# Performance work log

Measured on AMD Instinct MI355X. Metric: run time of the kernel, lower is better.

The kernel has to match this reference:

```python
import jax, jax.numpy as jnp
import numpy as np

T, D, I, E, G, LG, K = 2048, 1024, 512, 32, 8, 4, 6
SI = 2 * I  # shared expert inter dim = n_shared_experts * inter_dim
ROUTE_SCALE = 1.0


def setup_inputs() -> dict:
    key = jax.random.key(0)
    ks = jax.random.split(key, 16)
    s = 0.02
    f = jnp.float32
    return {
        "x": jax.random.normal(ks[0], (T, D), f),
        "router_w": jax.random.normal(ks[1], (E, D), f) * s,
        "router_b": jax.random.normal(ks[2], (E,), f) * s,
        "W1": jax.random.normal(ks[3], (E, D, I), f) * s,
        "b1": jax.random.normal(ks[4], (E, I), f) * s,
        "W2": jax.random.normal(ks[5], (E, D, I), f) * s,
        "b2": jax.random.normal(ks[6], (E, I), f) * s,
        "W3": jax.random.normal(ks[7], (E, I, D), f) * s,
        "b3": jax.random.normal(ks[8], (E, D), f) * s,
        "sw1": jax.random.normal(ks[9], (D, SI), f) * s,
        "sb1": jax.random.normal(ks[10], (SI,), f) * s,
        "sw2": jax.random.normal(ks[11], (D, SI), f) * s,
        "sb2": jax.random.normal(ks[12], (SI,), f) * s,
        "sw3": jax.random.normal(ks[13], (SI, D), f) * s,
        "sb3": jax.random.normal(ks[14], (D,), f) * s,
    }


def _route(x, router_w, router_b):
    # Router: softmax scores (fp32), group-limited top-k.
    logits = x @ router_w.T + router_b                      # [T, E]
    scores = jax.nn.softmax(logits.astype(jnp.float32), axis=-1)
    original = scores
    sg = scores.reshape(x.shape[0], G, E // G)              # [T, G, E/G]
    # no router bias -> group score = sum of top-2 expert scores per group
    group_scores = jnp.sum(jax.lax.top_k(sg, 2)[0], axis=-1)  # [T, G]
    _, gidx = jax.lax.top_k(group_scores, LG)               # [T, LG]
    keep = jnp.zeros((x.shape[0], G), bool).at[jnp.arange(x.shape[0])[:, None], gidx].set(True)
    masked = jnp.where(keep[:, :, None], sg, -jnp.inf).reshape(x.shape[0], E)
    _, idx = jax.lax.top_k(masked, K)                       # [T, K]
    vals = jnp.take_along_axis(original, idx, axis=1) * ROUTE_SCALE
    return vals.astype(x.dtype), idx


def reference(x, router_w, router_b, W1, b1, W2, b2, W3, b3, sw1, sb1, sw2, sb2, sw3, sb3):
    vals, idx = _route(x, router_w, router_b)
    # dense gate matrix [T, E]; top-k indices per row are distinct
    gates = jnp.zeros((x.shape[0], E), x.dtype).at[jnp.arange(x.shape[0])[:, None], idx].set(vals)
    # routed experts: Expert(x) = W3 @ silu(w1(x) * w2(x))
    h1 = jnp.einsum('td,edi->tei', x, W1) + b1              # [T, E, I]
    h2 = jnp.einsum('td,edi->tei', x, W2) + b2
    h = jax.nn.silu(h1 * h2)
    y = jnp.einsum('tei,eid->td', h * gates[:, :, None], W3) + gates @ b3
    # shared expert
    z = jax.nn.silu((x @ sw1 + sb1) * (x @ sw2 + sb2)) @ sw3 + sb3
    return y + z
```

## Files before the change

### kernel.cpp

```cpp
#include <hip/hip_runtime.h>
#include <hip/hip_bf16.h>
#include <math.h>

#define T_CONST 2048
#define D_CONST 1024
#define I_CONST 512
#define SI_CONST 1024
#define E_CONST 32
#define G_CONST 8
#define LG_CONST 4
#define KSEL 6
#define BK 32

typedef __attribute__((ext_vector_type(8))) short short8;
typedef __attribute__((ext_vector_type(4))) float floatx4;

__device__ inline unsigned pack_bf16(float a, float b) {
  __hip_bfloat162 h = __float22bfloat162_rn(float2{a, b});
  return *reinterpret_cast<unsigned*>(&h);
}

__device__ inline void gload16(const void* g, void* l) {
  __builtin_amdgcn_global_load_lds(
      (const __attribute__((address_space(1))) unsigned int*)g,
      (__attribute__((address_space(3))) unsigned int*)l, 16, 0, 0);
}

__global__ __launch_bounds__(256) void prep_all(
    const float* __restrict__ x, const float* __restrict__ rw,
    const float* __restrict__ W1, const float* __restrict__ W2,
    const float* __restrict__ W3, const float* __restrict__ sw1,
    const float* __restrict__ sw2, const float* __restrict__ sw3,
    __hip_bfloat16* __restrict__ x_bf, float* __restrict__ rwt,
    __hip_bfloat16* __restrict__ W1t, __hip_bfloat16* __restrict__ W2t,
    __hip_bfloat16* __restrict__ W3t, __hip_bfloat16* __restrict__ sw1t,
    __hip_bfloat16* __restrict__ sw2t, __hip_bfloat16* __restrict__ sw3t) {
  const int b = blockIdx.x;
  const int tid = threadIdx.x;
  if (b >= 3264) {
    int lb = b - 3264;
    if (lb < 512) {
      size_t base = (size_t)lb * 4096 + tid * 4;
#pragma unroll
      for (int it = 0; it < 4; ++it) {
        float4 v = *(const float4*)&x[base + it * 1024];
        uint2 u{pack_bf16(v.x, v.y), pack_bf16(v.z, v.w)};
        *(uint2*)&x_bf[base + it * 1024] = u;
      }
    } else {
      int lb2 = lb - 512;
#pragma unroll
      for (int it = 0; it < 4; ++it) {
        int i = lb2 * 1024 + it * 256 + tid;
        int d = i >> 5, e = i & 31;
        rwt[d * 32 + e] = rw[e * D_CONST + d];
      }
    }
    return;
  }
  const float* in;
  __hip_bfloat16* out;
  int K, N, k0, n0;
  if (b < 2048) {
    int mat = b >> 5, rem = b & 31;
    K = 1024; N = 512;
    int e = mat & 31;
    in = ((mat < 32) ? W1 : W2) + (size_t)e * (1024 * 512);
    out = ((mat < 32) ? W1t : W2t) + (size_t)e * (1024 * 512);
    k0 = (rem >> 3) * 256; n0 = (rem & 7) * 64;
  } else if (b < 3072) {
    int local = b - 2048;
    int e = local >> 5, rem = local & 31;
    K = 512; N = 1024;
    in = W3 + (size_t)e * (512 * 1024);
    out = W3t + (size_t)e * (512 * 1024);
    k0 = (rem >> 4) * 256; n0 = (rem & 15) * 64;
  } else {
    int local = b - 3072;
    int which = local >> 6, rem = local & 63;
    K = 1024; N = 1024;
    in = which == 0 ? sw1 : which == 1 ? sw2 : sw3;
    out = which == 0 ? sw1t : which == 1 ? sw2t : sw3t;
    k0 = (rem >> 4) * 256; n0 = (rem & 15) * 64;
  }
  __shared__ short tile[64 * 256];
  const int u = tid & 15, tr = tid >> 4;
#pragma unroll
  for (int sub = 0; sub < 4; ++sub) {
    float4 v[4];
#pragma unroll
    for (int r = 0; r < 4; ++r)
      v[r] = *(const float4*)&in[(size_t)(k0 + sub * 64 + 4 * tr + r) * N + n0 + 4 * u];
    int kb = sub * 64 + 4 * tr;
    int chunk = kb >> 3, half = (kb >> 2) & 1;
#pragma unroll
    for (int j = 0; j < 4; ++j) {
      int n = 4 * u + j;
      unsigned lo = pack_bf16(((const float*)&v[0])[j], ((const float*)&v[1])[j]);
      unsigned hi = pack_bf16(((const float*)&v[2])[j], ((const float*)&v[3])[j]);
      int cx = chunk ^ ((n >> 2) & 7) ^ ((n & 3) << 3);
      *(uint2*)&tile[n * 256 + cx * 8 + half * 4] = uint2{lo, hi};
    }
  }
  __syncthreads();
  const int n_ = tid >> 5, c_ = tid & 31;
#pragma unroll
  for (int p = 0; p < 8; ++p) {
    int n = p * 8 + n_;
    int cx = c_ ^ ((n >> 2) & 7) ^ ((n & 3) << 3);
    uint4 o = *(const uint4*)&tile[n * 256 + cx * 8];
    *(uint4*)&out[(size_t)(n0 + n) * K + k0 + c_ * 8] = o;
  }
}

__global__ __launch_bounds__(256) void router2(
    const float* __restrict__ x, const float* __restrict__ rwt,
    const float* __restrict__ rb, int* __restrict__ counts,
    int* __restrict__ stok, float* __restrict__ gatel) {
  const int lane = threadIdx.x & 63;
  const int wv = threadIdx.x >> 6;
  const int t = blockIdx.x * 4 + wv;
  const int e = lane & 31, h = lane >> 5;
  const float* xp = x + (size_t)t * D_CONST;
  float s = 0.f;
#pragma unroll 8
  for (int d = h; d < D_CONST; d += 2) s = fmaf(xp[d], rwt[d * 32 + e], s);
  s += __shfl_xor(s, 32);
  s += rb[e];
  float mx = s;
#pragma unroll
  for (int m = 16; m >= 1; m >>= 1) mx = fmaxf(mx, __shfl_xor(mx, m));
  float p = expf(s - mx);
  float sum = p;
#pragma unroll
  for (int m = 16; m >= 1; m >>= 1) sum += __shfl_xor(sum, m);
  float sc = p / sum;
  float a = sc, bb = __shfl_xor(a, 1);
  float hi = fmaxf(a, bb), lo = fminf(a, bb);
  float oh = __shfl_xor(hi, 2), ol = __shfl_xor(lo, 2);
  float gs = fmaxf(fmaxf(hi + oh, hi + lo), oh + ol);
  const int g = e >> 2;
  unsigned keep = 0;
  float gv = gs;
#pragma unroll
  for (int r = 0; r < LG_CONST; ++r) {
    float v = gv;
    int gi = g;
#pragma unroll
    for (int m = 16; m >= 1; m >>= 1) {
      float ov = __shfl_xor(v, m);
      int og = __shfl_xor(gi, m);
      if (ov > v || (ov == v && og < gi)) { v = ov; gi = og; }
    }
    keep |= 1u << gi;
    if (g == gi) gv = -1e30f;
  }
  float cand = ((keep >> g) & 1u) ? sc : -1e30f;
  int sel_e = -1;
  float sel_v = 0.f;
#pragma unroll
  for (int r = 0; r < KSEL; ++r) {
    float v = cand;
    int ei = e;
#pragma unroll
    for (int m = 16; m >= 1; m >>= 1) {
      float ov = __shfl_xor(v, m);
      int oe = __shfl_xor(ei, m);
      if (ov > v || (ov == v && oe < ei)) { v = ov; ei = oe; }
    }
    if (lane == r) { sel_e = ei; sel_v = v; }
    if (e == ei) cand = -1e30f;
  }
  if (lane < KSEL) {
    int pos = atomicAdd(&counts[sel_e], 1);
    stok[sel_e * T_CONST + pos] = t;
    gatel[sel_e * T_CONST + pos] = sel_v;
  }
}

__global__ __launch_bounds__(64) void plan_build(
    const int* __restrict__ counts, int* __restrict__ offsets,
    int* __restrict__ plan_up, int* __restrict__ plan_dn, int* __restrict__ meta) {
  const int lane = threadIdx.x;
  for (int i = lane; i < 128; i += 64) {
    int ent = (E_CONST << 8) | i;
    plan_up[i] = ent;
    plan_dn[i] = ent;
  }
  int cnt = (lane < E_CONST) ? counts[lane] : 0;
  int incl = cnt;
#pragma unroll
  for (int d = 1; d < 64; d <<= 1) {
    int v = __shfl_up(incl, d);
    if (lane >= d) incl += v;
  }
  if (lane < E_CONST) offsets[lane] = incl - cnt;
  if (lane == E_CONST - 1) offsets[E_CONST] = incl;
  int mbs = (cnt + 127) >> 7;
  int pm = mbs;
#pragma unroll
  for (int d = 1; d < 64; d <<= 1) {
    int v = __shfl_up(pm, d);
    if (lane >= d) pm += v;
  }
  int pmex = pm - mbs;
  if (lane < E_CONST) {
    int ub = 128 + pmex * 4, db = 128 + pmex * 8;
    for (int mb = 0; mb < mbs; ++mb) {
#pragma unroll
      for (int nb = 0; nb < 4; ++nb)
        plan_up[ub + mb * 4 + nb] = (lane << 8) | (mb << 3) | nb;
#pragma unroll
      for (int nb = 0; nb < 8; ++nb)
        plan_dn[db + mb * 8 + nb] = (lane << 8) | (mb << 3) | nb;
    }
  }
  if (lane == E_CONST - 1) {
    meta[0] = 128 + pm * 4;
    meta[1] = 128 + pm * 8;
  }
}

__global__ __launch_bounds__(256) void gather_x(
    const __hip_bfloat16* __restrict__ xbf, const int* __restrict__ counts,
    const int* __restrict__ offsets, const int* __restrict__ stok,
    const float* __restrict__ gatel, __hip_bfloat16* __restrict__ Xg,
    float* __restrict__ cgate, int* __restrict__ tcnt, int* __restrict__ tslot) {
  int e = blockIdx.x;
  int cnt = counts[e];
  int row = blockIdx.y * 16 + (threadIdx.x >> 4);
  if (row >= cnt) return;
  int seg = threadIdx.x & 15;
  int tok = stok[e * T_CONST + row];
  int dst = offsets[e] + row;
  const uint4* src = (const uint4*)(xbf + (size_t)tok * D_CONST);
  uint4* d = (uint4*)(Xg + (size_t)dst * D_CONST);
#pragma unroll
  for (int i = 0; i < 8; ++i) d[i * 16 + seg] = src[i * 16 + seg];
  if (seg == 0) {
    cgate[dst] = gatel[e * T_CONST + row];
    int sl = atomicAdd(&tcnt[tok], 1);
    tslot[tok * 8 + sl] = dst;
  }
}

__global__ __launch_bounds__(256, 2) void up_fused(
    const __hip_bfloat16* __restrict__ Xg, const __hip_bfloat16* __restrict__ xbf,
    const __hip_bfloat16* __restrict__ W1t, const __hip_bfloat16* __restrict__ W2t,
    const __hip_bfloat16* __restrict__ sw1t, const __hip_bfloat16* __restrict__ sw2t,
    const float* __restrict__ b1, const float* __restrict__ b2,
    const float* __restrict__ sb1, const float* __restrict__ sb2,
    const int* __restrict__ counts, const int* __restrict__ offsets,
    const int* __restrict__ plan, const int* __restrict__ meta,
    __hip_bfloat16* __restrict__ He, __hip_bfloat16* __restrict__ Hs) {
  const int nw = meta[0];
  const int bx = blockIdx.x;
  if (bx >= nw) return;
  const int q = nw >> 3, r = nw & 7, c = bx & 7, sl = bx >> 3;
  const int j = (c < r ? c * (q + 1) : r * (q + 1) + (c - r) * q) + sl;
  const int ent = plan[j];
  const int z = ent >> 8;
  const int m0 = ((ent >> 3) & 31) * 128;
  const int n0 = (ent & 7) * 128;
  const bool SH = (z == E_CONST);
  const int cnt = SH ? T_CONST : counts[z];
  const int base = SH ? 0 : offsets[z];

  const __hip_bfloat16* Ab = SH ? (xbf + (size_t)m0 * D_CONST)
                                : (Xg + (size_t)(base + m0) * D_CONST);
  const __hip_bfloat16* B1 = SH ? (sw1t + (size_t)n0 * D_CONST)
                                : (W1t + ((size_t)z * I_CONST + n0) * D_CONST);
  const __hip_bfloat16* B2 = SH ? (sw2t + (size_t)n0 * D_CONST)
                                : (W2t + ((size_t)z * I_CONST + n0) * D_CONST);

  __shared__ short As[3 * 4096], Bs1[3 * 4096], Bs2[3 * 4096];

  const int tid = threadIdx.x, lane = tid & 63, wv = tid >> 6;
  const int l15 = lane & 15, quad = lane >> 4;
  const int wm = wv & 1, wn = wv >> 1;
  const int lr = lane >> 2;
  const int lc = lane & 3;

  const __hip_bfloat16 *aG[2], *b1G[2], *b2G[2];
#pragma unroll
  for (int i = 0; i < 2; ++i) {
    int rr = wv * 32 + i * 16 + lr;
    int kap = lc ^ ((rr >> 1) & 3);
    aG[i]  = Ab + (size_t)rr * D_CONST + kap * 8;
    b1G[i] = B1 + (size_t)rr * D_CONST + kap * 8;
    b2G[i] = B2 + (size_t)rr * D_CONST + kap * 8;
  }
  const int ldsu = wv * 1024 + lane * 8;

  floatx4 acc1[4][4] = {};
  floatx4 acc2[4][4] = {};

  const int nIter = D_CONST / BK;

  auto stage = [&](int slot, int kk) {
    const int sb = slot * 4096;
#pragma unroll
    for (int i = 0; i < 2; ++i) {
      gload16(aG[i] + kk,  &As [sb + ldsu + i * 512]);
      gload16(b1G[i] + kk, &Bs1[sb + ldsu + i * 512]);
      gload16(b2G[i] + kk, &Bs2[sb + ldsu + i * 512]);
    }
  };

  stage(0, 0);
  stage(1, BK);
  int sl0 = 0, sl1 = 1, sl2 = 2;

  for (int s = 0; s < nIter; ++s) {
    int kn = (s + 2 < nIter) ? (s + 2) * BK : (nIter - 1) * BK;
    stage(sl2, kn);
    asm volatile("s_waitcnt vmcnt(12)" ::: "memory");
    __builtin_amdgcn_s_barrier();
    const int sb = sl0 * 4096;
    short8 a[4], x1[4], x2[4];
#pragma unroll
    for (int mi = 0; mi < 4; ++mi) {
      int m = wm * 64 + mi * 16 + l15;
      a[mi] = *(const short8*)&As[sb + m * 32 + (quad ^ ((m >> 1) & 3)) * 8];
    }
#pragma unroll
    for (int ni = 0; ni < 4; ++ni) {
      int n = wn * 64 + ni * 16 + l15;
      int uo = sb + n * 32 + (quad ^ ((n >> 1) & 3)) * 8;
      x1[ni] = *(const short8*)&Bs1[uo];
      x2[ni] = *(const short8*)&Bs2[uo];
    }
    __builtin_amdgcn_s_setprio(1);
#pragma unroll
    for (int mi = 0; mi < 4; ++mi)
#pragma unroll
      for (int ni = 0; ni < 4; ++ni) {
        acc1[mi][ni] = __builtin_amdgcn_mfma_f32_16x16x32_bf16(a[mi], x1[ni], acc1[mi][ni], 0, 0, 0);
        acc2[mi][ni] = __builtin_amdgcn_mfma_f32_16x16x32_bf16(a[mi], x2[ni], acc2[mi][ni], 0, 0, 0);
      }
    __builtin_amdgcn_s_setprio(0);
    __builtin_amdgcn_s_barrier();
    int t = sl0; sl0 = sl1; sl1 = sl2; sl2 = t;
  }
  asm volatile("s_waitcnt vmcnt(0)" ::: "memory");

  const float* pb1 = SH ? sb1 : (b1 + (size_t)z * I_CONST);
  const float* pb2 = SH ? sb2 : (b2 + (size_t)z * I_CONST);
  __hip_bfloat16* outp = SH ? (Hs + (size_t)m0 * SI_CONST + n0)
                            : (He + (size_t)(base + m0) * I_CONST + n0);
  const int ldo = SH ? SI_CONST : I_CONST;
  float c1[4], c2[4];
#pragma unroll
  for (int ni = 0; ni < 4; ++ni) {
    int n = wn * 64 + ni * 16 + l15;
    c1[ni] = pb1[n0 + n];
    c2[ni] = pb2[n0 + n];
  }
#pragma unroll
  for (int mi = 0; mi < 4; ++mi) {
#pragma unroll
    for (int reg = 0; reg < 4; ++reg) {
      int m = wm * 64 + mi * 16 + quad * 4 + reg;
      if (m0 + m >= cnt) continue;
#pragma unroll
      for (int ni = 0; ni < 4; ++ni) {
        int n = wn * 64 + ni * 16 + l15;
        float h1 = acc1[mi][ni][reg] + c1[ni];
        float h2 = acc2[mi][ni][reg] + c2[ni];
        float p = h1 * h2;
        float sg = p / (1.f + expf(-p));
        outp[(size_t)m * ldo + n] = __float2bfloat16(sg);
      }
    }
  }
}

__global__ __launch_bounds__(256, 3) void down_fused(
    const __hip_bfloat16* __restrict__ He, const __hip_bfloat16* __restrict__ Hs,
    const __hip_bfloat16* __restrict__ W3t, const __hip_bfloat16* __restrict__ sw3t,
    const float* __restrict__ b3, const float* __restrict__ sb3,
    const int* __restrict__ counts, const int* __restrict__ offsets,
    const float* __restrict__ cgate, const int* __restrict__ plan,
    const int* __restrict__ meta, float* __restrict__ Yp, float* __restrict__ out) {
  if ((int)blockIdx.x >= meta[1]) return;
  const int ent = plan[blockIdx.x];
  const int z = ent >> 8;
  const int m0 = ((ent >> 3) & 31) * 128;
  const int n0 = (ent & 7) * 128;
  const bool SH = (z == E_CONST);
  const int cnt = SH ? T_CONST : counts[z];
  const int base = SH ? 0 : offsets[z];
  const int Kd = SH ? SI_CONST : I_CONST;

  const __hip_bfloat16* Ab = SH ? (Hs + (size_t)m0 * SI_CONST)
                                : (He + (size_t)(base + m0) * I_CONST);
  const __hip_bfloat16* Bb = SH ? (sw3t + (size_t)n0 * SI_CONST)
                                : (W3t + ((size_t)z * D_CONST + n0) * I_CONST);

  __shared__ short As[2 * 4096], Bs[2 * 4096];

  const int tid = threadIdx.x, lane = tid & 63, wv = tid >> 6;
  const int l15 = lane & 15, quad = lane >> 4;
  const int wm = wv & 1, wn = wv >> 1;
  const int lr = lane >> 2, lc = lane & 3;

  const __hip_bfloat16 *aG[2], *bG[2];
#pragma unroll
  for (int i = 0; i < 2; ++i) {
    int rr = wv * 32 + i * 16 + lr;
    int kap = lc ^ ((rr >> 1) & 3);
    aG[i] = Ab + (size_t)rr * Kd + kap * 8;
    bG[i] = Bb + (size_t)rr * Kd + kap * 8;
  }
  const int ldsu = wv * 1024 + lane * 8;

  floatx4 acc[4][4] = {};
  const int nIter = Kd / BK;

  auto stage = [&](int slot, int kk) {
    const int sb = slot * 4096;
#pragma unroll
    for (int i = 0; i < 2; ++i) {
      gload16(aG[i] + kk, &As[sb + ldsu + i * 512]);
      gload16(bG[i] + kk, &Bs[sb + ldsu + i * 512]);
    }
  };

  stage(0, 0);
  int cur = 0;

  for (int s = 0; s < nIter; ++s) {
    int kn = (s + 1 < nIter) ? (s + 1) * BK : s * BK;
    stage(cur ^ 1, kn);
    asm volatile("s_waitcnt vmcnt(4)" ::: "memory");
    __builtin_amdgcn_s_barrier();
    const int sb = cur * 4096;
    short8 a[4], bbf[4];
#pragma unroll
    for (int mi = 0; mi < 4; ++mi) {
      int m = wm * 64 + mi * 16 + l15;
      a[mi] = *(const short8*)&As[sb + m * 32 + (quad ^ ((m >> 1) & 3)) * 8];
    }
#pragma unroll
    for (int ni = 0; ni < 4; ++ni) {
      int n = wn * 64 + ni * 16 + l15;
      bbf[ni] = *(const short8*)&Bs[sb + n * 32 + (quad ^ ((n >> 1) & 3)) * 8];
    }
    __builtin_amdgcn_s_setprio(1);
#pragma unroll
    for (int mi = 0; mi < 4; ++mi)
#pragma unroll
      for (int ni = 0; ni < 4; ++ni)
        acc[mi][ni] = __builtin_amdgcn_mfma_f32_16x16x32_bf16(a[mi], bbf[ni], acc[mi][ni], 0, 0, 0);
    __builtin_amdgcn_s_setprio(0);
    __builtin_amdgcn_s_barrier();
    cur ^= 1;
  }
  asm volatile("s_waitcnt vmcnt(0)" ::: "memory");

  float bias[4];
#pragma unroll
  for (int ni = 0; ni < 4; ++ni) {
    int n = n0 + wn * 64 + ni * 16 + l15;
    bias[ni] = SH ? sb3[n] : b3[(size_t)z * D_CONST + n];
  }
#pragma unroll
  for (int mi = 0; mi < 4; ++mi) {
#pragma unroll
    for (int reg = 0; reg < 4; ++reg) {
      int m = wm * 64 + mi * 16 + quad * 4 + reg;
      if (m0 + m >= cnt) continue;
#pragma unroll
      for (int ni = 0; ni < 4; ++ni) {
        int n = n0 + wn * 64 + ni * 16 + l15;
        float v = acc[mi][ni][reg] + bias[ni];
        if (SH) {
          out[(size_t)(m0 + m) * D_CONST + n] = v;
        } else {
          int grow = base + m0 + m;
          Yp[(size_t)grow * D_CONST + n] = cgate[grow] * v;
        }
      }
    }
  }
}

__global__ __launch_bounds__(256) void combine(
    const float* __restrict__ Yp, const int* __restrict__ tslot,
    float* __restrict__ out) {
  const int t = blockIdx.x;
  const int d = threadIdx.x * 4;
  const int* ts = &tslot[t * 8];
  float4 o = *(const float4*)&out[(size_t)t * D_CONST + d];
#pragma unroll
  for (int k = 0; k < KSEL; ++k) {
    float4 y = *(const float4*)&Yp[(size_t)ts[k] * D_CONST + d];
    o.x += y.x; o.y += y.y; o.z += y.z; o.w += y.w;
  }
  *(float4*)&out[(size_t)t * D_CONST + d] = o;
}

extern "C" void kernel_launch(void* const* d_in, const int* in_sizes, int n_in,
                              void* d_out, int out_size, void* d_ws, size_t ws_size,
                              hipStream_t stream) {
  const float* x   = (const float*)d_in[0];
  const float* rw  = (const float*)d_in[1];
  const float* rb  = (const float*)d_in[2];
  const float* W1  = (const float*)d_in[3];
  const float* b1  = (const float*)d_in[4];
  const float* W2  = (const float*)d_in[5];
  const float* b2  = (const float*)d_in[6];
  const float* W3  = (const float*)d_in[7];
  const float* b3  = (const float*)d_in[8];
  const float* sw1 = (const float*)d_in[9];
  const float* sb1 = (const float*)d_in[10];
  const float* sw2 = (const float*)d_in[11];
  const float* sb2 = (const float*)d_in[12];
  const float* sw3 = (const float*)d_in[13];
  const float* sb3 = (const float*)d_in[14];
  float* out = (float*)d_out;

  char* w = (char*)d_ws;
  size_t off = 0;
  auto alloc = [&](size_t bytes) {
    char* p = w + off;
    off += (bytes + 255) & ~(size_t)255;
    return p;
  };
  int* counts = (int*)alloc(E_CONST * 4);
  int* offsets = (int*)alloc((E_CONST + 1) * 4);
  int* meta = (int*)alloc(16);
  int* plan_up = (int*)alloc(768 * 4);
  int* plan_dn = (int*)alloc(1280 * 4);
  int* tcnt = (int*)alloc((size_t)T_CONST * 4);
  int* tslot = (int*)alloc((size_t)T_CONST * 8 * 4);
  int* stok = (int*)alloc((size_t)E_CONST * T_CONST * 4);
  float* gatel = (float*)alloc((size_t)E_CONST * T_CONST * 4);
  float* rwt = (float*)alloc((size_t)D_CONST * E_CONST * 4);
  float* cgate = (float*)alloc((size_t)T_CONST * KSEL * 4);
  __hip_bfloat16* x_bf = (__hip_bfloat16*)alloc((size_t)T_CONST * D_CONST * 2);
  __hip_bfloat16* Xg = (__hip_bfloat16*)alloc((size_t)(T_CONST * KSEL + 128) * D_CONST * 2);
  __hip_bfloat16* W1t = (__hip_bfloat16*)alloc((size_t)E_CONST * D_CONST * I_CONST * 2);
  __hip_bfloat16* W2t = (__hip_bfloat16*)alloc((size_t)E_CONST * D_CONST * I_CONST * 2);
  __hip_bfloat16* W3t = (__hip_bfloat16*)alloc((size_t)E_CONST * I_CONST * D_CONST * 2);
  __hip_bfloat16* sw1t = (__hip_bfloat16*)alloc((size_t)D_CONST * SI_CONST * 2);
  __hip_bfloat16* sw2t = (__hip_bfloat16*)alloc((size_t)D_CONST * SI_CONST * 2);
  __hip_bfloat16* sw3t = (__hip_bfloat16*)alloc((size_t)SI_CONST * D_CONST * 2);
  __hip_bfloat16* He = (__hip_bfloat16*)alloc((size_t)(T_CONST * KSEL + 128) * I_CONST * 2);
  __hip_bfloat16* Hs = (__hip_bfloat16*)alloc((size_t)T_CONST * SI_CONST * 2);
  float* Yp = (float*)W1t;

  hipMemsetAsync(counts, 0, E_CONST * sizeof(int), stream);
  hipMemsetAsync(tcnt, 0, (size_t)T_CONST * sizeof(int), stream);
  prep_all<<<3808, 256, 0, stream>>>(x, rw, W1, W2, W3, sw1, sw2, sw3,
                                     x_bf, rwt, W1t, W2t, W3t, sw1t, sw2t, sw3t);
  router2<<<T_CONST / 4, 256, 0, stream>>>(x, rwt, rb, counts, stok, gatel);
  plan_build<<<1, 64, 0, stream>>>(counts, offsets, plan_up, plan_dn, meta);
  gather_x<<<dim3(E_CONST, T_CONST / 16), 256, 0, stream>>>(
      x_bf, counts, offsets, stok, gatel, Xg, cgate, tcnt, tslot);
  up_fused<<<768, 256, 0, stream>>>(
      Xg, x_bf, W1t, W2t, sw1t, sw2t, b1, b2, sb1, sb2, counts, offsets,
      plan_up, meta, He, Hs);
  down_fused<<<1280, 256, 0, stream>>>(
      He, Hs, W3t, sw3t, b3, sb3, counts, offsets, cgate, plan_dn, meta, Yp, out);
  combine<<<T_CONST, 256, 0, stream>>>(Yp, tslot, out);
}
```

Before: 459.4 us.

## Use 8-wave 512-thread blocks for up and down GEMM kernels

Doubles the block size of the up and down expert GEMM kernels from 4 to 8 waves while keeping the 128x128 output tile. Each wave now computes 64x32 instead of 64x64, which halves the accumulator registers. Each thread issues a single global-to-LDS load per operand per stage, and the vmcnt waits are adjusted to match. The intent is more resident waves per CU to hide memory latency. The trade-off is less register-level reuse of A fragments, since each A fragment now feeds only two MFMAs per operand, and more barrier participants per block.

```diff
diff --git a/kernel.cpp b/kernel.cpp
--- a/kernel.cpp
+++ b/kernel.cpp
@@ -244,7 +244,7 @@
   }
 }
 
-__global__ __launch_bounds__(256, 2) void up_fused(
+__global__ __launch_bounds__(512, 4) void up_fused(
     const __hip_bfloat16* __restrict__ Xg, const __hip_bfloat16* __restrict__ xbf,
     const __hip_bfloat16* __restrict__ W1t, const __hip_bfloat16* __restrict__ W2t,
     const __hip_bfloat16* __restrict__ sw1t, const __hip_bfloat16* __restrict__ sw2t,
@@ -278,33 +278,25 @@
   const int tid = threadIdx.x, lane = tid & 63, wv = tid >> 6;
   const int l15 = lane & 15, quad = lane >> 4;
   const int wm = wv & 1, wn = wv >> 1;
-  const int lr = lane >> 2;
-  const int lc = lane & 3;
-
-  const __hip_bfloat16 *aG[2], *b1G[2], *b2G[2];
-#pragma unroll
-  for (int i = 0; i < 2; ++i) {
-    int rr = wv * 32 + i * 16 + lr;
-    int kap = lc ^ ((rr >> 1) & 3);
-    aG[i]  = Ab + (size_t)rr * D_CONST + kap * 8;
-    b1G[i] = B1 + (size_t)rr * D_CONST + kap * 8;
-    b2G[i] = B2 + (size_t)rr * D_CONST + kap * 8;
-  }
-  const int ldsu = wv * 1024 + lane * 8;
-
-  floatx4 acc1[4][4] = {};
-  floatx4 acc2[4][4] = {};
+  const int srow = tid >> 2;
+  const int slc = tid & 3;
+  const int kap = slc ^ ((srow >> 1) & 3);
+
+  const __hip_bfloat16* aG  = Ab + (size_t)srow * D_CONST + kap * 8;
+  const __hip_bfloat16* b1G = B1 + (size_t)srow * D_CONST + kap * 8;
+  const __hip_bfloat16* b2G = B2 + (size_t)srow * D_CONST + kap * 8;
+  const int ldsu = tid * 8;
+
+  floatx4 acc1[4][2] = {};
+  floatx4 acc2[4][2] = {};
 
   const int nIter = D_CONST / BK;
 
   auto stage = [&](int slot, int kk) {
     const int sb = slot * 4096;
-#pragma unroll
-    for (int i = 0; i < 2; ++i) {
-      gload16(aG[i] + kk,  &As [sb + ldsu + i * 512]);
-      gload16(b1G[i] + kk, &Bs1[sb + ldsu + i * 512]);
-      gload16(b2G[i] + kk, &Bs2[sb + ldsu + i * 512]);
-    }
+    gload16(aG + kk,  &As [sb + ldsu]);
+    gload16(b1G + kk, &Bs1[sb + ldsu]);
+    gload16(b2G + kk, &Bs2[sb + ldsu]);
   };
 
   stage(0, 0);
@@ -314,30 +306,28 @@
   for (int s = 0; s < nIter; ++s) {
     int kn = (s + 2 < nIter) ? (s + 2) * BK : (nIter - 1) * BK;
     stage(sl2, kn);
-    asm volatile("s_waitcnt vmcnt(12)" ::: "memory");
+    asm volatile("s_waitcnt vmcnt(6)" ::: "memory");
     __builtin_amdgcn_s_barrier();
     const int sb = sl0 * 4096;
-    short8 a[4], x1[4], x2[4];
-#pragma unroll
-    for (int mi = 0; mi < 4; ++mi) {
-      int m = wm * 64 + mi * 16 + l15;
-      a[mi] = *(const short8*)&As[sb + m * 32 + (quad ^ ((m >> 1) & 3)) * 8];
-    }
-#pragma unroll
-    for (int ni = 0; ni < 4; ++ni) {
-      int n = wn * 64 + ni * 16 + l15;
+    short8 x1[2], x2[2];
+#pragma unroll
+    for (int ni = 0; ni < 2; ++ni) {
+      int n = wn * 32 + ni * 16 + l15;
       int uo = sb + n * 32 + (quad ^ ((n >> 1) & 3)) * 8;
       x1[ni] = *(const short8*)&Bs1[uo];
       x2[ni] = *(const short8*)&Bs2[uo];
     }
     __builtin_amdgcn_s_setprio(1);
 #pragma unroll
-    for (int mi = 0; mi < 4; ++mi)
-#pragma unroll
-      for (int ni = 0; ni < 4; ++ni) {
-        acc1[mi][ni] = __builtin_amdgcn_mfma_f32_16x16x32_bf16(a[mi], x1[ni], acc1[mi][ni], 0, 0, 0);
-        acc2[mi][ni] = __builtin_amdgcn_mfma_f32_16x16x32_bf16(a[mi], x2[ni], acc2[mi][ni], 0, 0, 0);
+    for (int mi = 0; mi < 4; ++mi) {
+      int m = wm * 64 + mi * 16 + l15;
+      short8 a = *(const short8*)&As[sb + m * 32 + (quad ^ ((m >> 1) & 3)) * 8];
+#pragma unroll
+      for (int ni = 0; ni < 2; ++ni) {
+        acc1[mi][ni] = __builtin_amdgcn_mfma_f32_16x16x32_bf16(a, x1[ni], acc1[mi][ni], 0, 0, 0);
+        acc2[mi][ni] = __builtin_amdgcn_mfma_f32_16x16x32_bf16(a, x2[ni], acc2[mi][ni], 0, 0, 0);
       }
+    }
     __builtin_amdgcn_s_setprio(0);
     __builtin_amdgcn_s_barrier();
     int t = sl0; sl0 = sl1; sl1 = sl2; sl2 = t;
@@ -349,10 +339,10 @@
   __hip_bfloat16* outp = SH ? (Hs + (size_t)m0 * SI_CONST + n0)
                             : (He + (size_t)(base + m0) * I_CONST + n0);
   const int ldo = SH ? SI_CONST : I_CONST;
-  float c1[4], c2[4];
-#pragma unroll
-  for (int ni = 0; ni < 4; ++ni) {
-    int n = wn * 64 + ni * 16 + l15;
+  float c1[2], c2[2];
+#pragma unroll
+  for (int ni = 0; ni < 2; ++ni) {
+    int n = wn * 32 + ni * 16 + l15;
     c1[ni] = pb1[n0 + n];
     c2[ni] = pb2[n0 + n];
   }
@@ -363,8 +353,8 @@
       int m = wm * 64 + mi * 16 + quad * 4 + reg;
       if (m0 + m >= cnt) continue;
 #pragma unroll
-      for (int ni = 0; ni < 4; ++ni) {
-        int n = wn * 64 + ni * 16 + l15;
+      for (int ni = 0; ni < 2; ++ni) {
+        int n = wn * 32 + ni * 16 + l15;
         float h1 = acc1[mi][ni][reg] + c1[ni];
         float h2 = acc2[mi][ni][reg] + c2[ni];
         float p = h1 * h2;
@@ -375,7 +365,7 @@
   }
 }
 
-__global__ __launch_bounds__(256, 3) void down_fused(
+__global__ __launch_bounds__(512, 4) void down_fused(
     const __hip_bfloat16* __restrict__ He, const __hip_bfloat16* __restrict__ Hs,
     const __hip_bfloat16* __restrict__ W3t, const __hip_bfloat16* __restrict__ sw3t,
     const float* __restrict__ b3, const float* __restrict__ sb3,
@@ -402,28 +392,20 @@
   const int tid = threadIdx.x, lane = tid & 63, wv = tid >> 6;
   const int l15 = lane & 15, quad = lane >> 4;
   const int wm = wv & 1, wn = wv >> 1;
-  const int lr = lane >> 2, lc = lane & 3;
-
-  const __hip_bfloat16 *aG[2], *bG[2];
-#pragma unroll
-  for (int i = 0; i < 2; ++i) {
-    int rr = wv * 32 + i * 16 + lr;
-    int kap = lc ^ ((rr >> 1) & 3);
-    aG[i] = Ab + (size_t)rr * Kd + kap * 8;
-    bG[i] = Bb + (size_t)rr * Kd + kap * 8;
-  }
-  const int ldsu = wv * 1024 + lane * 8;
-
-  floatx4 acc[4][4] = {};
+  const int srow = tid >> 2, slc = tid & 3;
+  const int kap = slc ^ ((srow >> 1) & 3);
+
+  const __hip_bfloat16* aG = Ab + (size_t)srow * Kd + kap * 8;
+  const __hip_bfloat16* bG = Bb + (size_t)srow * Kd + kap * 8;
+  const int ldsu = tid * 8;
+
+  floatx4 acc[4][2] = {};
   const int nIter = Kd / BK;
 
   auto stage = [&](int slot, int kk) {
     const int sb = slot * 4096;
-#pragma unroll
-    for (int i = 0; i < 2; ++i) {
-      gload16(aG[i] + kk, &As[sb + ldsu + i * 512]);
-      gload16(bG[i] + kk, &Bs[sb + ldsu + i * 512]);
-    }
+    gload16(aG + kk, &As[sb + ldsu]);
+    gload16(bG + kk, &Bs[sb + ldsu]);
   };
 
   stage(0, 0);
@@ -432,36 +414,34 @@
   for (int s = 0; s < nIter; ++s) {
     int kn = (s + 1 < nIter) ? (s + 1) * BK : s * BK;
     stage(cur ^ 1, kn);
-    asm volatile("s_waitcnt vmcnt(4)" ::: "memory");
+    asm volatile("s_waitcnt vmcnt(2)" ::: "memory");
     __builtin_amdgcn_s_barrier();
     const int sb = cur * 4096;
-    short8 a[4], bbf[4];
+    short8 bb[2];
+#pragma unroll
+    for (int ni = 0; ni < 2; ++ni) {
+      int n = wn * 32 + ni * 16 + l15;
+      bb[ni] = *(const short8*)&Bs[sb + n * 32 + (quad ^ ((n >> 1) & 3)) * 8];
+    }
+    __builtin_amdgcn_s_setprio(1);
 #pragma unroll
     for (int mi = 0; mi < 4; ++mi) {
       int m = wm * 64 + mi * 16 + l15;
-      a[mi] = *(const short8*)&As[sb + m * 32 + (quad ^ ((m >> 1) & 3)) * 8];
-    }
-#pragma unroll
-    for (int ni = 0; ni < 4; ++ni) {
-      int n = wn * 64 + ni * 16 + l15;
-      bbf[ni] = *(const short8*)&Bs[sb + n * 32 + (quad ^ ((n >> 1) & 3)) * 8];
-    }
-    __builtin_amdgcn_s_setprio(1);
-#pragma unroll
-    for (int mi = 0; mi < 4; ++mi)
-#pragma unroll
-      for (int ni = 0; ni < 4; ++ni)
-        acc[mi][ni] = __builtin_amdgcn_mfma_f32_16x16x32_bf16(a[mi], bbf[ni], acc[mi][ni], 0, 0, 0);
+      short8 a = *(const short8*)&As[sb + m * 32 + (quad ^ ((m >> 1) & 3)) * 8];
+#pragma unroll
+      for (int ni = 0; ni < 2; ++ni)
+        acc[mi][ni] = __builtin_amdgcn_mfma_f32_16x16x32_bf16(a, bb[ni], acc[mi][ni], 0, 0, 0);
+    }
     __builtin_amdgcn_s_setprio(0);
     __builtin_amdgcn_s_barrier();
     cur ^= 1;
   }
   asm volatile("s_waitcnt vmcnt(0)" ::: "memory");
 
-  float bias[4];
-#pragma unroll
-  for (int ni = 0; ni < 4; ++ni) {
-    int n = n0 + wn * 64 + ni * 16 + l15;
+  float bias[2];
+#pragma unroll
+  for (int ni = 0; ni < 2; ++ni) {
+    int n = n0 + wn * 32 + ni * 16 + l15;
     bias[ni] = SH ? sb3[n] : b3[(size_t)z * D_CONST + n];
   }
 #pragma unroll
@@ -471,8 +451,8 @@
       int m = wm * 64 + mi * 16 + quad * 4 + reg;
       if (m0 + m >= cnt) continue;
 #pragma unroll
-      for (int ni = 0; ni < 4; ++ni) {
-        int n = n0 + wn * 64 + ni * 16 + l15;
+      for (int ni = 0; ni < 2; ++ni) {
+        int n = n0 + wn * 32 + ni * 16 + l15;
         float v = acc[mi][ni][reg] + bias[ni];
         if (SH) {
           out[(size_t)(m0 + m) * D_CONST + n] = v;
@@ -558,10 +538,10 @@
   plan_build<<<1, 64, 0, stream>>>(counts, offsets, plan_up, plan_dn, meta);
   gather_x<<<dim3(E_CONST, T_CONST / 16), 256, 0, stream>>>(
       x_bf, counts, offsets, stok, gatel, Xg, cgate, tcnt, tslot);
-  up_fused<<<768, 256, 0, stream>>>(
+  up_fused<<<768, 512, 0, stream>>>(
       Xg, x_bf, W1t, W2t, sw1t, sw2t, b1, b2, sb1, sb2, counts, offsets,
       plan_up, meta, He, Hs);
-  down_fused<<<1280, 256, 0, stream>>>(
+  down_fused<<<1280, 512, 0, stream>>>(
       He, Hs, W3t, sw3t, b3, sb3, counts, offsets, cgate, plan_dn, meta, Yp, out);
   combine<<<T_CONST, 256, 0, stream>>>(Yp, tslot, out);
 }
```

Measured after the change: 448.9 us. -2.3%, faster.
